# Kernel tuning notes

Hardware: AMD Instinct MI355X
Metric: run time of the kernel (lower is better)

## Reference

```python
import jax, jax.numpy as jnp
import numpy as np

D_MODEL = 2048
NUM_HEADS = 16
D_K = D_MODEL // NUM_HEADS


def setup_inputs() -> dict:
    key = jax.random.key(0)
    ks = jax.random.split(key, 9)
    s = 1.0 / np.sqrt(D_MODEL)
    x = jax.random.normal(ks[0], (4, 4096, D_MODEL), dtype=jnp.float32)
    wq = jax.random.uniform(ks[1], (D_MODEL, D_MODEL), jnp.float32, -s, s)
    bq = jax.random.uniform(ks[2], (D_MODEL,), jnp.float32, -s, s)
    wk = jax.random.uniform(ks[3], (D_MODEL, D_MODEL), jnp.float32, -s, s)
    bk = jax.random.uniform(ks[4], (D_MODEL,), jnp.float32, -s, s)
    wv = jax.random.uniform(ks[5], (D_MODEL, D_MODEL), jnp.float32, -s, s)
    bv = jax.random.uniform(ks[6], (D_MODEL,), jnp.float32, -s, s)
    wo = jax.random.uniform(ks[7], (D_MODEL, D_MODEL), jnp.float32, -s, s)
    bo = jax.random.uniform(ks[8], (D_MODEL,), jnp.float32, -s, s)
    return {"x": x, "wq": wq, "bq": bq, "wk": wk, "bk": bk,
            "wv": wv, "bv": bv, "wo": wo, "bo": bo}


def _heads(t, B, S):
    # (B, S, d_model) -> (B, H, S, d_k)
    return t.reshape(B, S, NUM_HEADS, D_K).transpose(0, 2, 1, 3)


def reference(x, wq, bq, wk, bk, wv, bv, wo, bo):
    B, S, _ = x.shape
    Q = _heads(x @ wq.T + bq, B, S)
    K = _heads(x @ wk.T + bk, B, S)
    V = _heads(x @ wv.T + bv, B, S)
    # elu(x)+1 feature map
    Q = jax.nn.elu(Q) + 1.0
    K = jax.nn.elu(K) + 1.0
    # KV: (B,H,d_k,d_k)
    KV = jnp.einsum('bhsd,bhse->bhde', K, V)
    QKV = jnp.einsum('bhsd,bhde->bhse', Q, KV)
    K_sum = jnp.sum(K, axis=-2)                      # (B,H,d_k)
    QK_sum = jnp.einsum('bhsd,bhd->bhs', Q, K_sum)   # (B,H,S)
    out = QKV / (QK_sum[..., None] + 1e-8)
    out = out.transpose(0, 2, 1, 3).reshape(B, S, D_MODEL)
    return out @ wo.T + bo
```

## Files before the change

### kernel.cpp

```cpp
#include <hip/hip_runtime.h>


#define D_MODEL 2048
#define SEQ     4096
#define BATCH   4
#define HEADS   16
#define DKH     128
#define M_TOK   16384
#define NBH     64

using frag8 = __attribute__((ext_vector_type(8))) short;
using f32x4 = __attribute__((ext_vector_type(4))) float;

typedef __attribute__((address_space(1))) const unsigned int g_u32;
typedef __attribute__((address_space(3))) unsigned int       l_u32;

__device__ __forceinline__ unsigned short f2bf(float f) {
  unsigned u = __float_as_uint(f);
  u = u + 0x7fffu + ((u >> 16) & 1u);
  return (unsigned short)(u >> 16);
}
__device__ __forceinline__ float bf2f(unsigned short h) {
  return __uint_as_float(((unsigned)h) << 16);
}

__global__ __launch_bounds__(256) void convert_f2bf_kernel(
    const float* __restrict__ in, unsigned short* __restrict__ out, int n4) {
  int i = blockIdx.x * 256 + threadIdx.x;
  if (i < n4) {
    float4 v = reinterpret_cast<const float4*>(in)[i];
    ushort4 o;
    o.x = f2bf(v.x); o.y = f2bf(v.y); o.z = f2bf(v.z); o.w = f2bf(v.w);
    reinterpret_cast<ushort4*>(out)[i] = o;
  }
}


__device__ __forceinline__ void stage_group(const unsigned short* __restrict__ GA, long lda,
                                            const unsigned short* __restrict__ GB, long ldb,
                                            int kcol, unsigned short* __restrict__ Ldst,
                                            int wid, int lane) {
  const int quad = (lane & 7) ^ (lane >> 3);
  const int rr   = (quad >> 2) * 128 + wid * 16 + (lane >> 3);
  const int col  = kcol + (quad & 3) * 8;
#pragma unroll
  for (int j = 0; j < 2; ++j)
    __builtin_amdgcn_global_load_lds((g_u32*)(GA + (long)(rr + j * 8) * lda + col),
                                     (l_u32*)(Ldst + (wid * 128 + j * 64) * 8), 16, 0, 0);
#pragma unroll
  for (int j = 0; j < 2; ++j)
    __builtin_amdgcn_global_load_lds((g_u32*)(GB + (long)(rr + j * 8) * ldb + col),
                                     (l_u32*)(Ldst + 8192 + (wid * 128 + j * 64) * 8), 16, 0, 0);
}

#define DS_AV2(LA, MS)                                                        \
  _Pragma("unroll") for (int i_ = 0; i_ < 4; ++i_) {                          \
    const int p_ = (MS) * 64 + i_ * 16 + lr;                                  \
    const int q_ = (wm * 4 + lh) ^ (lr & 7);                                  \
    av[i_] = *(const frag8*)((LA) + p_ * 64 + q_ * 8);                        \
  }
#define DS_BV2(LB)                                                            \
  _Pragma("unroll") for (int n_ = 0; n_ < 4; ++n_) {                          \
    const int p_ = (wn & 1) * 64 + n_ * 16 + lr;                              \
    const int q_ = ((wn >> 1) * 4 + lh) ^ (lr & 7);                           \
    bv[n_] = *(const frag8*)((LB) + p_ * 64 + q_ * 8);                        \
  }
#define MFMA16(MS)                                                            \
  __builtin_amdgcn_s_setprio(1);                                              \
  _Pragma("unroll") for (int i_ = 0; i_ < 4; ++i_)                            \
  _Pragma("unroll") for (int n_ = 0; n_ < 4; ++n_)                            \
    acc[(MS) * 4 + i_][n_] = __builtin_amdgcn_mfma_f32_16x16x32_bf16(         \
        av[i_], bv[n_], acc[(MS) * 4 + i_][n_], 0, 0, 0);                     \
  __builtin_amdgcn_s_setprio(0);
#define LGKM0                                                                 \
  asm volatile("s_waitcnt lgkmcnt(0)" ::: "memory");                          \
  __builtin_amdgcn_sched_barrier(0)
#define BARRIER                                                               \
  __builtin_amdgcn_s_barrier();                                               \
  __builtin_amdgcn_sched_barrier(0)

template <int MODE, bool XMAJOR>
__global__ __launch_bounds__(512, 2) void gemm256_nt_kernel(
    const unsigned short* __restrict__ A, long lda,
    const unsigned short* __restrict__ Bm, long ldb,
    void* __restrict__ Cv, long ldc,
    const float* __restrict__ bias, int K) {
  __shared__ unsigned short sh[65536];
  const int lane = threadIdx.x & 63, wid = threadIdx.x >> 6;
  const int wm = wid >> 2, wn = wid & 3;
  const int lr = lane & 15, lh = lane >> 4;

  const int gx = gridDim.x, gy = gridDim.y;
  const int cpx = (gx * gy) >> 3;
  const int P = blockIdx.y * gx + blockIdx.x;
  const int Lw = (P & 7) * cpx + (P >> 3);
  int bx, by;
  if (XMAJOR) { bx = Lw / gy; by = Lw - bx * gy; }
  else        { by = Lw / gx; bx = Lw - by * gx; }

  const long m0 = (long)by * 256, n0 = (long)bx * 256;
  const unsigned short* Ablk = A + m0 * lda;
  const unsigned short* Bblk = Bm + n0 * ldb;
  const int NT = K >> 6;

  f32x4 acc[8][4];
#pragma unroll
  for (int m = 0; m < 8; ++m)
#pragma unroll
    for (int n = 0; n < 4; ++n) acc[m][n] = (f32x4){0.f, 0.f, 0.f, 0.f};

  stage_group(Ablk, lda, Bblk, ldb, 0,  (unsigned short*)sh,         wid, lane);
  stage_group(Ablk, lda, Bblk, ldb, 32, (unsigned short*)sh + 16384, wid, lane);
  if (NT > 1) {
    stage_group(Ablk, lda, Bblk, ldb, 64, (unsigned short*)sh + 32768, wid, lane);
    stage_group(Ablk, lda, Bblk, ldb, 96, (unsigned short*)sh + 49152, wid, lane);
  }
  asm volatile("s_waitcnt vmcnt(12)" ::: "memory");
  BARRIER;

  for (int t = 0; t < NT; ++t) {
    const int sl0 = (t & 1) * 2;
    const unsigned short* lA0 = sh + sl0 * 16384;
    const unsigned short* lB0 = lA0 + 8192;
    const unsigned short* lA1 = lA0 + 16384;
    const unsigned short* lB1 = lA1 + 8192;
    frag8 av[4], bv[4];
    DS_AV2(lA0, 0); DS_BV2(lB0);
    LGKM0; MFMA16(0);
    DS_AV2(lA0, 1);
    LGKM0;
    if (t < NT - 1) asm volatile("s_waitcnt vmcnt(8)" ::: "memory");
    else            asm volatile("s_waitcnt vmcnt(0)" ::: "memory");
    BARRIER;
    if (t + 2 < NT)
      stage_group(Ablk, lda, Bblk, ldb, (t + 2) * 64,
                  (unsigned short*)sh + sl0 * 16384, wid, lane);
    MFMA16(1);
    DS_AV2(lA1, 0); DS_BV2(lB1);
    LGKM0; MFMA16(0);
    DS_AV2(lA1, 1);
    LGKM0;
    if (t < NT - 1) {
      if (t < NT - 2) asm volatile("s_waitcnt vmcnt(8)" ::: "memory");
      else            asm volatile("s_waitcnt vmcnt(4)" ::: "memory");
      BARRIER;
      if (t + 2 < NT)
        stage_group(Ablk, lda, Bblk, ldb, (t + 2) * 64 + 32,
                    (unsigned short*)sh + (sl0 + 1) * 16384, wid, lane);
    }
    MFMA16(1);
  }

#pragma unroll
  for (int m = 0; m < 8; ++m)
#pragma unroll
    for (int n = 0; n < 4; ++n)
#pragma unroll
      for (int r = 0; r < 4; ++r) {
        long row = m0 + wm * 128 + (m >> 2) * 64 + (m & 3) * 16 + lh * 4 + r;
        long col = n0 + wn * 64 + n * 16 + lr;
        float v = acc[m][n][r];
        if (MODE == 0) {
          v += bias[col]; v = v > 0.f ? v + 1.f : __expf(v);
          ((unsigned short*)Cv)[row * ldc + col] = f2bf(v);
        } else if (MODE == 1) {
          v += bias[row]; v = v > 0.f ? v + 1.f : __expf(v);
          ((unsigned short*)Cv)[row * ldc + col] = f2bf(v);
        } else if (MODE == 2) {
          v += bias[row];
          ((unsigned short*)Cv)[row * ldc + col] = f2bf(v);
        } else {
          v += bias[col];
          ((float*)Cv)[row * ldc + col] = v;
        }
      }
}

__device__ __forceinline__ void stage_tile(const unsigned short* __restrict__ G,
                                           long ld, unsigned short* __restrict__ L) {
  const int w = threadIdx.x >> 6, l = threadIdx.x & 63;
#pragma unroll
  for (int r = 0; r < 4; ++r) {
    const int chunk = w * 4 + r;
    const int row = chunk * 8 + (l >> 3);
    const int col = (l & 7) * 8;
    __builtin_amdgcn_global_load_lds((g_u32*)(G + (long)row * ld + col),
                                     (l_u32*)(L + chunk * 512), 16, 0, 0);
  }
}

__device__ __forceinline__ void gemm_mainloop(const unsigned short* __restrict__ A, long lda,
                                              const unsigned short* __restrict__ B, long ldb,
                                              int K, unsigned short* lA, unsigned short* lB,
                                              f32x4 acc[4][4]) {
  const int lane = threadIdx.x & 63;
  const int wid  = threadIdx.x >> 6;
  const int wr = wid >> 1, wc = wid & 1;
  const int lr = lane & 15, lh = lane >> 4;
  for (int k0 = 0; k0 < K; k0 += 64) {
    stage_tile(A + k0, lda, lA);
    stage_tile(B + k0, ldb, lB);
    __syncthreads();
#pragma unroll
    for (int kk = 0; kk < 64; kk += 32) {
      frag8 av[4], bv[4];
#pragma unroll
      for (int m = 0; m < 4; ++m)
        av[m] = *reinterpret_cast<const frag8*>(lA + (wr * 64 + m * 16 + lr) * 64 + kk + lh * 8);
#pragma unroll
      for (int n = 0; n < 4; ++n)
        bv[n] = *reinterpret_cast<const frag8*>(lB + (wc * 64 + n * 16 + lr) * 64 + kk + lh * 8);
#pragma unroll
      for (int m = 0; m < 4; ++m)
#pragma unroll
        for (int n = 0; n < 4; ++n)
          acc[m][n] = __builtin_amdgcn_mfma_f32_16x16x32_bf16(av[m], bv[n], acc[m][n], 0, 0, 0);
    }
    __syncthreads();
  }
}

#define ACC_INIT(acc)                                   \
  _Pragma("unroll") for (int m_ = 0; m_ < 4; ++m_)      \
  _Pragma("unroll") for (int n_ = 0; n_ < 4; ++n_)      \
      acc[m_][n_] = (f32x4){0.f, 0.f, 0.f, 0.f};

__global__ __launch_bounds__(256) void kvt_partial_kernel(
    const unsigned short* __restrict__ VT, const unsigned short* __restrict__ KT,
    float* __restrict__ part) {
  __shared__ unsigned short lA[128 * 64], lB[128 * 64];
  const int z = blockIdx.x;
  const int bh = z >> 3, c = z & 7;
  const int b = bh >> 4, h = bh & 15;
  const long tOff = (long)b * SEQ + (long)c * 512;
  const unsigned short* A  = VT + (long)(h * DKH) * M_TOK + tOff;
  const unsigned short* Bm = KT + (long)(h * DKH) * M_TOK + tOff;
  f32x4 acc[4][4];
  ACC_INIT(acc);
  gemm_mainloop(A, M_TOK, Bm, M_TOK, 512, lA, lB, acc);
  const int lane = threadIdx.x & 63, wid = threadIdx.x >> 6;
  const int wr = wid >> 1, wc = wid & 1, lr = lane & 15, lh = lane >> 4;
  float* out = part + (long)z * (DKH * DKH);
#pragma unroll
  for (int m = 0; m < 4; ++m)
#pragma unroll
    for (int n = 0; n < 4; ++n)
#pragma unroll
      for (int r = 0; r < 4; ++r) {
        int row = wr * 64 + m * 16 + lh * 4 + r;
        int col = wc * 64 + n * 16 + lr;
        out[row * DKH + col] = acc[m][n][r];
      }
}

__global__ __launch_bounds__(256) void reduce_kvt_kernel(
    const float* __restrict__ part, unsigned short* __restrict__ kvt) {
  int i = blockIdx.x * 256 + threadIdx.x;
  if (i < NBH * DKH * DKH) {
    int bh = i >> 14, j = i & 16383;
    float s = 0.f;
#pragma unroll
    for (int c = 0; c < 8; ++c) s += part[(((long)bh * 8 + c) << 14) + j];
    kvt[i] = f2bf(s);
  }
}

__global__ __launch_bounds__(256) void ksum_kernel(const unsigned short* __restrict__ KT,
                                                   float* __restrict__ ksum) {
  int gr = blockIdx.x * 4 + (threadIdx.x >> 6);
  int lane = threadIdx.x & 63;
  int bh = gr >> 7, d = gr & 127;
  int b = bh >> 4, h = bh & 15;
  const unsigned short* p = KT + (long)(h * DKH + d) * M_TOK + (long)b * SEQ;
  float s = 0.f;
#pragma unroll
  for (int i = 0; i < 8; ++i) {
    uint4 v = *reinterpret_cast<const uint4*>(p + (i * 64 + lane) * 8);
    unsigned w[4] = {v.x, v.y, v.z, v.w};
#pragma unroll
    for (int j = 0; j < 4; ++j) {
      s += bf2f((unsigned short)(w[j] & 0xffff));
      s += bf2f((unsigned short)(w[j] >> 16));
    }
  }
#pragma unroll
  for (int o = 32; o > 0; o >>= 1) s += __shfl_down(s, o);
  if (lane == 0) ksum[gr] = s;
}

__global__ __launch_bounds__(256) void qsum_kernel(const unsigned short* __restrict__ Q,
                                                   const float* __restrict__ ksum,
                                                   float* __restrict__ qsum) {
  int gr = blockIdx.x * 4 + (threadIdx.x >> 6);
  int lane = threadIdx.x & 63;
  int bh = gr >> 12, s = gr & 4095;
  int b = bh >> 4, h = bh & 15;
  const unsigned short* q = Q + ((long)b * SEQ + s) * D_MODEL + h * DKH + lane * 2;
  unsigned u = *reinterpret_cast<const unsigned*>(q);
  const float* ks = ksum + bh * DKH + lane * 2;
  float sum = bf2f((unsigned short)(u & 0xffff)) * ks[0] +
              bf2f((unsigned short)(u >> 16)) * ks[1];
#pragma unroll
  for (int o = 32; o > 0; o >>= 1) sum += __shfl_down(sum, o);
  if (lane == 0) qsum[gr] = sum;
}

__global__ __launch_bounds__(256) void qkv_kernel(const unsigned short* __restrict__ Q,
                                                  const unsigned short* __restrict__ KVT,
                                                  const float* __restrict__ qsum,
                                                  unsigned short* __restrict__ attn) {
  __shared__ unsigned short lA[128 * 64], lB[128 * 64];
  const int z = blockIdx.z, b = z >> 4, h = z & 15;
  const long m0 = (long)blockIdx.y * 128;
  const unsigned short* A  = Q + ((long)b * SEQ + m0) * D_MODEL + h * DKH;
  const unsigned short* Bm = KVT + (long)z * (DKH * DKH);
  f32x4 acc[4][4];
  ACC_INIT(acc);
  gemm_mainloop(A, D_MODEL, Bm, DKH, DKH, lA, lB, acc);
  const int lane = threadIdx.x & 63, wid = threadIdx.x >> 6;
  const int wr = wid >> 1, wc = wid & 1, lr = lane & 15, lh = lane >> 4;
#pragma unroll
  for (int m = 0; m < 4; ++m)
#pragma unroll
    for (int n = 0; n < 4; ++n)
#pragma unroll
      for (int r = 0; r < 4; ++r) {
        long row = m0 + wr * 64 + m * 16 + lh * 4 + r;
        int  col = wc * 64 + n * 16 + lr;
        float dnm = qsum[(long)z * SEQ + row] + 1e-8f;
        float v = acc[m][n][r] / dnm;
        attn[((long)b * SEQ + row) * D_MODEL + h * DKH + col] = f2bf(v);
      }
}

#define OFF_XB   0L
#define OFF_WQ   (OFF_XB + (long)M_TOK * D_MODEL * 2)
#define OFF_WK   (OFF_WQ + (long)D_MODEL * D_MODEL * 2)
#define OFF_WV   (OFF_WK + (long)D_MODEL * D_MODEL * 2)
#define OFF_WO   (OFF_WV + (long)D_MODEL * D_MODEL * 2)
#define OFF_QB   (OFF_WO + (long)D_MODEL * D_MODEL * 2)
#define OFF_KT   (OFF_QB + (long)M_TOK * D_MODEL * 2)
#define OFF_VT   (OFF_KT + (long)M_TOK * D_MODEL * 2)
#define OFF_PART (OFF_VT + (long)M_TOK * D_MODEL * 2)
#define OFF_KVT  (OFF_PART + (long)512 * DKH * DKH * 4)
#define OFF_KSUM (OFF_KVT + (long)NBH * DKH * DKH * 2)
#define OFF_QSUM (OFF_KSUM + (long)NBH * DKH * 4)
#define OFF_ATTN OFF_XB

extern "C" void kernel_launch(void* const* d_in, const int* in_sizes, int n_in,
                              void* d_out, int out_size, void* d_ws, size_t ws_size,
                              hipStream_t stream) {
  const float* x  = (const float*)d_in[0];
  const float* wq = (const float*)d_in[1];
  const float* bq = (const float*)d_in[2];
  const float* wk = (const float*)d_in[3];
  const float* bk = (const float*)d_in[4];
  const float* wv = (const float*)d_in[5];
  const float* bv = (const float*)d_in[6];
  const float* wo = (const float*)d_in[7];
  const float* bo = (const float*)d_in[8];

  char* ws = (char*)d_ws;
  unsigned short* xb   = (unsigned short*)(ws + OFF_XB);
  unsigned short* wqb  = (unsigned short*)(ws + OFF_WQ);
  unsigned short* wkb  = (unsigned short*)(ws + OFF_WK);
  unsigned short* wvb  = (unsigned short*)(ws + OFF_WV);
  unsigned short* wob  = (unsigned short*)(ws + OFF_WO);
  unsigned short* Qb   = (unsigned short*)(ws + OFF_QB);
  unsigned short* KTb  = (unsigned short*)(ws + OFF_KT);
  unsigned short* VTb  = (unsigned short*)(ws + OFF_VT);
  float*          part = (float*)(ws + OFF_PART);
  unsigned short* KVTb = (unsigned short*)(ws + OFF_KVT);
  float*          ksum = (float*)(ws + OFF_KSUM);
  float*          qsum = (float*)(ws + OFF_QSUM);
  unsigned short* attn = (unsigned short*)(ws + OFF_ATTN);

  dim3 blk(256);
  dim3 blk5(512);

  convert_f2bf_kernel<<<(M_TOK * D_MODEL / 4) / 256, blk, 0, stream>>>(x, xb, M_TOK * D_MODEL / 4);
  convert_f2bf_kernel<<<(D_MODEL * D_MODEL / 4) / 256, blk, 0, stream>>>(wq, wqb, D_MODEL * D_MODEL / 4);
  convert_f2bf_kernel<<<(D_MODEL * D_MODEL / 4) / 256, blk, 0, stream>>>(wk, wkb, D_MODEL * D_MODEL / 4);
  convert_f2bf_kernel<<<(D_MODEL * D_MODEL / 4) / 256, blk, 0, stream>>>(wv, wvb, D_MODEL * D_MODEL / 4);
  convert_f2bf_kernel<<<(D_MODEL * D_MODEL / 4) / 256, blk, 0, stream>>>(wo, wob, D_MODEL * D_MODEL / 4);

  gemm256_nt_kernel<0, false><<<dim3(D_MODEL / 256, M_TOK / 256), blk5, 0, stream>>>(
      xb, D_MODEL, wqb, D_MODEL, Qb, D_MODEL, bq, D_MODEL);
  gemm256_nt_kernel<1, true><<<dim3(M_TOK / 256, D_MODEL / 256), blk5, 0, stream>>>(
      wkb, D_MODEL, xb, D_MODEL, KTb, M_TOK, bk, D_MODEL);
  gemm256_nt_kernel<2, true><<<dim3(M_TOK / 256, D_MODEL / 256), blk5, 0, stream>>>(
      wvb, D_MODEL, xb, D_MODEL, VTb, M_TOK, bv, D_MODEL);

  kvt_partial_kernel<<<512, blk, 0, stream>>>(VTb, KTb, part);
  reduce_kvt_kernel<<<(NBH * DKH * DKH) / 256, blk, 0, stream>>>(part, KVTb);

  ksum_kernel<<<(NBH * DKH) / 4, blk, 0, stream>>>(KTb, ksum);
  qsum_kernel<<<(NBH * SEQ) / 4, blk, 0, stream>>>(Qb, ksum, qsum);

  qkv_kernel<<<dim3(1, SEQ / 128, NBH), blk, 0, stream>>>(Qb, KVTb, qsum, attn);

  gemm256_nt_kernel<3, false><<<dim3(D_MODEL / 256, M_TOK / 256), blk5, 0, stream>>>(
      attn, D_MODEL, wob, D_MODEL, d_out, D_MODEL, bo, D_MODEL);
}
```

Measured before the change: 701.4 us.

## Double-buffer LDS fragment registers to overlap ds_reads with MFMA in GEMM loop

Result: no change. 694.4 us (-1.0%).

```diff
diff --git a/kernel.cpp b/kernel.cpp
--- a/kernel.cpp
+++ b/kernel.cpp
@@ -53,31 +53,25 @@
                                      (l_u32*)(Ldst + 8192 + (wid * 128 + j * 64) * 8), 16, 0, 0);
 }
 
-#define DS_AV2(LA, MS)                                                        \
+#define DS_AV_TO(dst, LA, MS)                                                 \
   _Pragma("unroll") for (int i_ = 0; i_ < 4; ++i_) {                          \
     const int p_ = (MS) * 64 + i_ * 16 + lr;                                  \
     const int q_ = (wm * 4 + lh) ^ (lr & 7);                                  \
-    av[i_] = *(const frag8*)((LA) + p_ * 64 + q_ * 8);                        \
-  }
-#define DS_BV2(LB)                                                            \
+    dst[i_] = *(const frag8*)((LA) + p_ * 64 + q_ * 8);                       \
+  }
+#define DS_BV_TO(dst, LB)                                                     \
   _Pragma("unroll") for (int n_ = 0; n_ < 4; ++n_) {                          \
     const int p_ = (wn & 1) * 64 + n_ * 16 + lr;                              \
     const int q_ = ((wn >> 1) * 4 + lh) ^ (lr & 7);                           \
-    bv[n_] = *(const frag8*)((LB) + p_ * 64 + q_ * 8);                        \
-  }
-#define MFMA16(MS)                                                            \
+    dst[n_] = *(const frag8*)((LB) + p_ * 64 + q_ * 8);                       \
+  }
+#define MFMA16_AB(a_, b_, MS)                                                 \
   __builtin_amdgcn_s_setprio(1);                                              \
   _Pragma("unroll") for (int i_ = 0; i_ < 4; ++i_)                            \
   _Pragma("unroll") for (int n_ = 0; n_ < 4; ++n_)                            \
     acc[(MS) * 4 + i_][n_] = __builtin_amdgcn_mfma_f32_16x16x32_bf16(         \
-        av[i_], bv[n_], acc[(MS) * 4 + i_][n_], 0, 0, 0);                     \
+        a_[i_], b_[n_], acc[(MS) * 4 + i_][n_], 0, 0, 0);                     \
   __builtin_amdgcn_s_setprio(0);
-#define LGKM0                                                                 \
-  asm volatile("s_waitcnt lgkmcnt(0)" ::: "memory");                          \
-  __builtin_amdgcn_sched_barrier(0)
-#define BARRIER                                                               \
-  __builtin_amdgcn_s_barrier();                                               \
-  __builtin_amdgcn_sched_barrier(0)
 
 template <int MODE, bool XMAJOR>
 __global__ __launch_bounds__(512, 2) void gemm256_nt_kernel(
@@ -116,39 +110,42 @@
     stage_group(Ablk, lda, Bblk, ldb, 96, (unsigned short*)sh + 49152, wid, lane);
   }
   asm volatile("s_waitcnt vmcnt(12)" ::: "memory");
-  BARRIER;
+  __builtin_amdgcn_s_barrier();
+
+  frag8 avc[4], avn[4], bvc[4], bvn[4];
+  DS_AV_TO(avc, (const unsigned short*)sh, 0);
+  DS_BV_TO(bvc, (const unsigned short*)sh + 8192);
 
   for (int t = 0; t < NT; ++t) {
-    const int sl0 = (t & 1) * 2;
-    const unsigned short* lA0 = sh + sl0 * 16384;
-    const unsigned short* lB0 = lA0 + 8192;
-    const unsigned short* lA1 = lA0 + 16384;
-    const unsigned short* lB1 = lA1 + 8192;
-    frag8 av[4], bv[4];
-    DS_AV2(lA0, 0); DS_BV2(lB0);
-    LGKM0; MFMA16(0);
-    DS_AV2(lA0, 1);
-    LGKM0;
+    const unsigned short* sl0 = (const unsigned short*)sh + ((t & 1) * 2) * 16384;
+    const unsigned short* sl1 = sl0 + 16384;
+    const unsigned short* nsl = (const unsigned short*)sh + (((t + 1) & 1) * 2) * 16384;
+    DS_AV_TO(avn, sl0, 1);
+    MFMA16_AB(avc, bvc, 0);
+    asm volatile("s_waitcnt lgkmcnt(0)" ::: "memory");
     if (t < NT - 1) asm volatile("s_waitcnt vmcnt(8)" ::: "memory");
     else            asm volatile("s_waitcnt vmcnt(0)" ::: "memory");
-    BARRIER;
+    __builtin_amdgcn_s_barrier();
     if (t + 2 < NT)
       stage_group(Ablk, lda, Bblk, ldb, (t + 2) * 64,
-                  (unsigned short*)sh + sl0 * 16384, wid, lane);
-    MFMA16(1);
-    DS_AV2(lA1, 0); DS_BV2(lB1);
-    LGKM0; MFMA16(0);
-    DS_AV2(lA1, 1);
-    LGKM0;
+                  (unsigned short*)sl0, wid, lane);
+    DS_AV_TO(avc, sl1, 0);
+    DS_BV_TO(bvn, sl1 + 8192);
+    MFMA16_AB(avn, bvc, 1);
+    DS_AV_TO(avn, sl1, 1);
+    MFMA16_AB(avc, bvn, 0);
+    asm volatile("s_waitcnt lgkmcnt(0)" ::: "memory");
+    if (t < NT - 2)       asm volatile("s_waitcnt vmcnt(8)" ::: "memory");
+    else if (t == NT - 2) asm volatile("s_waitcnt vmcnt(4)" ::: "memory");
     if (t < NT - 1) {
-      if (t < NT - 2) asm volatile("s_waitcnt vmcnt(8)" ::: "memory");
-      else            asm volatile("s_waitcnt vmcnt(4)" ::: "memory");
-      BARRIER;
+      __builtin_amdgcn_s_barrier();
       if (t + 2 < NT)
         stage_group(Ablk, lda, Bblk, ldb, (t + 2) * 64 + 32,
-                    (unsigned short*)sh + (sl0 + 1) * 16384, wid, lane);
+                    (unsigned short*)sl1, wid, lane);
+      DS_AV_TO(avc, nsl, 0);
+      DS_BV_TO(bvc, nsl + 8192);
     }
-    MFMA16(1);
+    MFMA16_AB(avn, bvn, 1);
   }
 
 #pragma unroll
```
